# Kernel optimization log

Measured on AMD Instinct MI355X. Metric: run time of the kernel, lower is better.

Reference implementation:

```python
import jax, jax.numpy as jnp
import numpy as np
import math

EPS = 1e-8
DIM, HEADS, K = 256, 8, 16
HD = DIM // HEADS
B, N, PDIM = 4, 4096, 3


def _layernorm(x, w, b, eps=1e-5):
    m = jnp.mean(x, axis=-1, keepdims=True)
    v = jnp.mean((x - m) ** 2, axis=-1, keepdims=True)
    return (x - m) * jax.lax.rsqrt(v + eps) * w + b


def setup_inputs() -> dict:
    key = jax.random.key(0)
    ks = jax.random.split(key, 16)
    s = 0.02
    d = {
        'x': jax.random.normal(ks[0], (B, N, DIM), jnp.float32),
        'positions': jax.random.uniform(ks[1], (B, N, PDIM), jnp.float32) * 0.5,  # inside unit ball
        'c': jnp.ones((1,), jnp.float32),
        'time_emb': jax.random.normal(ks[2], (B, DIM), jnp.float32),
        'Wq': jax.random.normal(ks[3], (DIM, DIM), jnp.float32) * s,
        'bq': jnp.zeros((DIM,), jnp.float32),
        'Wk': jax.random.normal(ks[4], (DIM, DIM), jnp.float32) * s,
        'bk': jnp.zeros((DIM,), jnp.float32),
        'Wv': jax.random.normal(ks[5], (DIM, DIM), jnp.float32) * s,
        'bv': jnp.zeros((DIM,), jnp.float32),
        'Wo': jax.random.normal(ks[6], (DIM, DIM), jnp.float32) * s,
        'bo': jnp.zeros((DIM,), jnp.float32),
        'W1': jax.random.normal(ks[7], (DIM, 4 * DIM), jnp.float32) * s,
        'b1': jnp.zeros((4 * DIM,), jnp.float32),
        'W2': jax.random.normal(ks[8], (4 * DIM, DIM), jnp.float32) * s,
        'b2': jnp.zeros((DIM,), jnp.float32),
        'ln1_w': jnp.ones((DIM,), jnp.float32),
        'ln1_b': jnp.zeros((DIM,), jnp.float32),
        'ln2_w': jnp.ones((DIM,), jnp.float32),
        'ln2_b': jnp.zeros((DIM,), jnp.float32),
        'log_tau': jnp.zeros((), jnp.float32),
    }
    return d


def _poincare_dist_matrix(pos, c):
    # pos: [B,N,P], c: scalar > 0. Returns [B,N,N] with d[b,i,j] = dist(pos[b,j], pos[b,i])
    sq = jnp.sum(pos ** 2, axis=-1)                      # [B,N]
    diff2 = (sq[:, :, None] + sq[:, None, :]
             - 2.0 * jnp.einsum('bip,bjp->bij', pos, pos))
    diff2 = jnp.maximum(diff2, 0.0)
    num = 2.0 * c * diff2
    den = (1.0 - c * sq[:, :, None]) * (1.0 - c * sq[:, None, :])
    arg = jnp.maximum(1.0 + num / (den + EPS), 1.0)
    return jnp.arccosh(arg) / jnp.sqrt(c)


def reference(x, positions, c, time_emb, Wq, bq, Wk, bk, Wv, bv, Wo, bo,
              W1, b1, W2, b2, ln1_w, ln1_b, ln2_w, ln2_b, log_tau):
    c_s = jnp.squeeze(c)
    x_res = x
    h = _layernorm(x, ln1_w, ln1_b) + time_emb[:, None, :]

    q = (h @ Wq + bq).reshape(B, N, HEADS, HD).transpose(0, 2, 1, 3)  # [B,H,N,hd]
    k = (h @ Wk + bk).reshape(B, N, HEADS, HD).transpose(0, 2, 1, 3)
    v = (h @ Wv + bv).reshape(B, N, HEADS, HD).transpose(0, 2, 1, 3)

    # pairwise hyperbolic distances + kNN (no_grad in original)
    dist = jax.lax.stop_gradient(_poincare_dist_matrix(positions, c_s))  # [B,N,N]
    neg_vals, idx = jax.lax.top_k(-dist, K)          # smallest-K distances
    attn_dists = -neg_vals                            # [B,N,K]

    # gather neighbor keys/values: out[b,h,n,j,d] = k[b,h,idx[b,n,j],d]
    idx_flat = idx.reshape(B, 1, N * K, 1)            # broadcast over heads, hd
    k_g = jnp.take_along_axis(k, idx_flat, axis=2).reshape(B, HEADS, N, K, HD)
    v_g = jnp.take_along_axis(v, idx_flat, axis=2).reshape(B, HEADS, N, K, HD)

    feat = jnp.einsum('bhnd,bhnkd->bhnk', q, k_g) / math.sqrt(HD)
    tau = jnp.exp(log_tau) + EPS
    scores = feat - attn_dists[:, None, :, :] / tau
    probs = jax.nn.softmax(scores, axis=-1)
    attn = jnp.einsum('bhnk,bhnkd->bhnd', probs, v_g)
    attn = attn.transpose(0, 2, 1, 3).reshape(B, N, DIM)

    x2 = x_res + attn @ Wo + bo
    ff = jax.nn.gelu(_layernorm(x2, ln2_w, ln2_b) @ W1 + b1, approximate=False) @ W2 + b2
    return x2 + ff
```

## Files before the change

### kernel.cpp

```cpp
#include <hip/hip_runtime.h>
#include <math.h>

namespace {

constexpr int kBatch = 4;
constexpr int kN = 4096;
constexpr int kDim = 256;
constexpr int kHeads = 8;
constexpr int kK = 16;
constexpr float kEps = 1e-8f;

using u16 = unsigned short;
typedef __attribute__((ext_vector_type(8))) short short8;
typedef __attribute__((ext_vector_type(8))) u16 u16x8;
typedef __attribute__((ext_vector_type(4))) float f32x4;

__device__ __forceinline__ float b2f(u16 u) {
  union { unsigned int i; float f; } x; x.i = ((unsigned int)u) << 16; return x.f;
}
__device__ __forceinline__ u16 f2b(float f) {
  union { float f; unsigned int i; } x; x.f = f;
  unsigned int r = x.i + 0x7fffu + ((x.i >> 16) & 1u);
  return (u16)(r >> 16);
}
__device__ __forceinline__ float gelu_exact(float x) {
  return 0.5f * x * (1.0f + erff(x * 0.70710678118654752f));
}
__device__ __forceinline__ void load_lds16(const u16* g, u16* l) {
  __builtin_amdgcn_global_load_lds(
      (const __attribute__((address_space(1))) unsigned int*)g,
      (__attribute__((address_space(3))) unsigned int*)l, 16, 0, 0);
}

template<bool ADD_TEMB>
__global__ __launch_bounds__(256) void ln_kernel(
    const float* __restrict__ x, const float* __restrict__ w,
    const float* __restrict__ bb, const float* __restrict__ temb,
    u16* __restrict__ out) {
  int gt = blockIdx.x * 256 + threadIdx.x;
  int row = gt >> 6;
  int lane = threadIdx.x & 63;
  const float4* xr = (const float4*)(x + (size_t)row * kDim);
  float4 v = xr[lane];
  float s = v.x + v.y + v.z + v.w;
  #pragma unroll
  for (int off = 32; off; off >>= 1) s += __shfl_xor(s, off);
  float mean = s * (1.0f / kDim);
  float dx = v.x - mean, dy = v.y - mean, dz = v.z - mean, dw = v.w - mean;
  float ss = dx * dx + dy * dy + dz * dz + dw * dw;
  #pragma unroll
  for (int off = 32; off; off >>= 1) ss += __shfl_xor(ss, off);
  float rstd = rsqrtf(ss * (1.0f / kDim) + 1e-5f);
  float4 wv = ((const float4*)w)[lane];
  float4 bv = ((const float4*)bb)[lane];
  float ox = dx * rstd * wv.x + bv.x;
  float oy = dy * rstd * wv.y + bv.y;
  float oz = dz * rstd * wv.z + bv.z;
  float ow = dw * rstd * wv.w + bv.w;
  if (ADD_TEMB) {
    int bi = row >> 12;
    float4 t = ((const float4*)(temb + (size_t)bi * kDim))[lane];
    ox += t.x; oy += t.y; oz += t.z; ow += t.w;
  }
  ushort4 ob;
  ob.x = f2b(ox); ob.y = f2b(oy); ob.z = f2b(oz); ob.w = f2b(ow);
  ((ushort4*)(out + (size_t)row * kDim))[lane] = ob;
}

__global__ __launch_bounds__(256) void wconv_all_kernel(
    const float* __restrict__ Wq, const float* __restrict__ Wk,
    const float* __restrict__ Wv, const float* __restrict__ Wo,
    const float* __restrict__ W1, const float* __restrict__ W2,
    u16* __restrict__ Tq, u16* __restrict__ Tk,
    u16* __restrict__ Tv, u16* __restrict__ To,
    u16* __restrict__ T1, u16* __restrict__ T2) {
  int idx = blockIdx.x * 256 + threadIdx.x;
  int seg = idx >> 18;
  int e = idx & 262143;
  if (seg == 0) {
    int which = e >> 16, ee = e & 65535;
    const float* W = which == 0 ? Wq : which == 1 ? Wk : which == 2 ? Wv : Wo;
    u16* T = which == 0 ? Tq : which == 1 ? Tk : which == 2 ? Tv : To;
    int n = ee >> 8, kk = ee & 255;
    T[ee] = f2b(W[kk * 256 + n]);
  } else if (seg == 1) {
    int n = e >> 8, kk = e & 255;
    T1[e] = f2b(W1[kk * 1024 + n]);
  } else {
    int n = e >> 10, kk = e & 1023;
    T2[e] = f2b(W2[kk * 256 + n]);
  }
}

template<int EPI, int BN>
__device__ __forceinline__ void gemm_body(
    const u16* __restrict__ A, const u16* __restrict__ Bt,
    const float* __restrict__ bias, const float* __restrict__ R,
    float* __restrict__ Cf, u16* __restrict__ Cbf,
    int N, int K, int bx, int by) {
  constexpr int NI = BN / 32;
  __shared__ u16 Al[128 * 32];
  __shared__ u16 Bl[BN * 32];
  int tid = threadIdx.x;
  int wv = tid >> 6, ln = tid & 63;
  int wr = wv >> 1, wc = wv & 1;
  int lhi = ln >> 4, llo = ln & 15;
  int bm = bx * 128, bn = by * BN;

  f32x4 zero = {0.f, 0.f, 0.f, 0.f};
  f32x4 acc[4][NI];
  #pragma unroll
  for (int mi = 0; mi < 4; ++mi)
    #pragma unroll
    for (int ni = 0; ni < NI; ++ni) acc[mi][ni] = zero;

  for (int k0 = 0; k0 < K; k0 += 32) {
    if (k0) __syncthreads();
    #pragma unroll
    for (int i = 0; i < 2; ++i) {
      int f = i * 256 + tid;
      int r = f >> 2, kp = f & 3;
      load_lds16(A + (size_t)(bm + r) * K + k0 + kp * 8,
                 &Al[(i * 256 + wv * 64) * 8]);
    }
    #pragma unroll
    for (int i = 0; i < BN / 64; ++i) {
      int f = i * 256 + tid;
      int r = f >> 2, kp = f & 3;
      load_lds16(Bt + (size_t)(bn + r) * K + k0 + kp * 8,
                 &Bl[(i * 256 + wv * 64) * 8]);
    }
    __syncthreads();
    short8 af[4], bf[NI];
    #pragma unroll
    for (int mi = 0; mi < 4; ++mi)
      af[mi] = *(const short8*)&Al[(wr * 64 + mi * 16 + llo) * 32 + lhi * 8];
    #pragma unroll
    for (int ni = 0; ni < NI; ++ni)
      bf[ni] = *(const short8*)&Bl[(wc * (BN / 2) + ni * 16 + llo) * 32 + lhi * 8];
    #pragma unroll
    for (int mi = 0; mi < 4; ++mi)
      #pragma unroll
      for (int ni = 0; ni < NI; ++ni)
        acc[mi][ni] = __builtin_amdgcn_mfma_f32_16x16x32_bf16(
            af[mi], bf[ni], acc[mi][ni], 0, 0, 0);
  }

  #pragma unroll
  for (int mi = 0; mi < 4; ++mi) {
    #pragma unroll
    for (int r = 0; r < 4; ++r) {
      int row = bm + wr * 64 + mi * 16 + lhi * 4 + r;
      #pragma unroll
      for (int ni = 0; ni < NI; ++ni) {
        int col = bn + wc * (BN / 2) + ni * 16 + llo;
        float val = acc[mi][ni][r] + bias[col];
        if (EPI == 1) {
          val += R[(size_t)row * N + col];
          Cf[(size_t)row * N + col] = val;
        } else {
          if (EPI == 2) val = gelu_exact(val);
          Cbf[(size_t)row * N + col] = f2b(val);
        }
      }
    }
  }
}

template<int EPI, int BN>
__global__ __launch_bounds__(256) void gemm_kernel(
    const u16* __restrict__ A, const u16* __restrict__ Bt,
    const float* __restrict__ bias, const float* __restrict__ R,
    float* __restrict__ Cf, u16* __restrict__ Cbf, int N, int K) {
  gemm_body<EPI, BN>(A, Bt, bias, R, Cf, Cbf, N, K, blockIdx.x, blockIdx.y);
}

__global__ __launch_bounds__(256) void qkv_kernel(
    const u16* __restrict__ A,
    const u16* __restrict__ Bq, const u16* __restrict__ Bk, const u16* __restrict__ Bv,
    const float* __restrict__ bq, const float* __restrict__ bk, const float* __restrict__ bv,
    u16* __restrict__ q, u16* __restrict__ k, u16* __restrict__ v) {
  int sel = blockIdx.y >> 1;
  const u16* Bt = sel == 0 ? Bq : sel == 1 ? Bk : Bv;
  const float* bias = sel == 0 ? bq : sel == 1 ? bk : bv;
  u16* C = sel == 0 ? q : sel == 1 ? k : v;
  gemm_body<0, 128>(A, Bt, bias, nullptr, nullptr, C, 256, 256,
                    blockIdx.x, blockIdx.y & 1);
}

__global__ __launch_bounds__(1024, 4) void topk_kernel(
    const float* __restrict__ pos, const float* __restrict__ cptr,
    int* __restrict__ idx_out, float* __restrict__ dist_out) {
  __shared__ float4 ps[kN];
  int tid = threadIdx.x;
  int wave = tid >> 6, ln = tid & 63;
  int row = blockIdx.x * 16 + wave;
  int b = row >> 12;
  float c = cptr[0];
  const float4* pbv = (const float4*)(pos + (size_t)b * kN * 3);
  {
    int q = tid;
    float4 f0 = pbv[q * 3 + 0], f1 = pbv[q * 3 + 1], f2 = pbv[q * 3 + 2];
    float xs[4] = {f0.x, f0.w, f1.z, f2.y};
    float ys[4] = {f0.y, f1.x, f1.w, f2.z};
    float zs[4] = {f0.z, f1.y, f2.x, f2.w};
    #pragma unroll
    for (int e = 0; e < 4; ++e)
      ps[q * 4 + e] = make_float4(xs[e], ys[e], zs[e],
          c * (xs[e] * xs[e] + ys[e] * ys[e] + zs[e] * zs[e]));
  }
  __syncthreads();

  int i = row & (kN - 1);
  float4 pi = ps[i];
  float wi = pi.w, oi = 1.0f - wi;
  float sx = 2.0f * c * pi.x, sy = 2.0f * c * pi.y, sz = 2.0f * c * pi.z;

  auto pkey = [&](int j) -> unsigned {
    float4 pj = ps[j];
    float tt = wi + pj.w;
    tt = fmaf(-sx, pj.x, tt);
    tt = fmaf(-sy, pj.y, tt);
    tt = fmaf(-sz, pj.z, tt);
    float num = 2.0f * fmaxf(tt, 0.0f);
    float den = fmaf(-oi, pj.w, oi) + kEps;
    float r = num * __builtin_amdgcn_rcpf(den);
    union { float f; unsigned u; } cv; cv.f = r;
    return (cv.u & 0xFFFFF000u) | (unsigned)j;
  };

  unsigned lpk = pkey(ln);
  #pragma unroll
  for (int kk = 2; kk <= 64; kk <<= 1) {
    #pragma unroll
    for (int jj = kk >> 1; jj >= 1; jj >>= 1) {
      unsigned ov = (unsigned)__shfl_xor((int)lpk, jj);
      bool keepMin = (((ln & kk) == 0) == ((ln & jj) == 0));
      bool less = ov < lpk;
      if (keepMin ? less : !less) lpk = ov;
    }
  }
  unsigned T = (unsigned)__builtin_amdgcn_readlane((int)lpk, 15);

  for (int t = 1; t < 64; ++t) {
    unsigned cpk = pkey(ln + t * 64);
    unsigned long long m = __ballot(cpk < T);
    if (m) {
      do {
        int src = __ffsll(m) - 1;
        m &= m - 1;
        unsigned npk = (unsigned)__builtin_amdgcn_readlane((int)cpk, src);
        unsigned pv = (unsigned)__builtin_amdgcn_update_dpp(
            0, (int)lpk, 0x111 , 0xF, 0xF, false);
        bool gt = lpk > npk;
        bool take = gt && ((ln == 0) || (pv <= npk));
        lpk = take ? npk : (gt ? pv : lpk);
      } while (m);
      T = (unsigned)__builtin_amdgcn_readlane((int)lpk, 15);
    }
  }

  if (ln < kK) {
    int j = (int)(lpk & 0xFFFu);
    float4 pj = ps[j];
    float tt = wi + pj.w;
    tt = fmaf(-sx, pj.x, tt);
    tt = fmaf(-sy, pj.y, tt);
    tt = fmaf(-sz, pj.z, tt);
    float num = 2.0f * fmaxf(tt, 0.0f);
    float den = fmaf(-oi, pj.w, oi) + kEps;
    float arg = fmaxf(1.0f + num / den, 1.0f);
    float rs = 1.0f / sqrtf(c);
    idx_out[(size_t)row * kK + ln] = j;
    dist_out[(size_t)row * kK + ln] = acoshf(arg) * rs;
  }
}

__global__ __launch_bounds__(256) void attn_kernel(
    const u16* __restrict__ q, const u16* __restrict__ k,
    const u16* __restrict__ v, const int* __restrict__ nidx,
    const float* __restrict__ ndist, const float* __restrict__ log_tau,
    u16* __restrict__ out) {
  int t = blockIdx.x * 256 + threadIdx.x;
  int h = t & (kHeads - 1);
  int row = t >> 3;
  int b = row >> 12;
  float rtau = 1.0f / (expf(log_tau[0]) + kEps);
  const u16x8* qr = (const u16x8*)(q + (size_t)row * kDim + h * 32);
  float qf[32];
  #pragma unroll
  for (int cch = 0; cch < 4; ++cch) {
    u16x8 u = qr[cch];
    #pragma unroll
    for (int e = 0; e < 8; ++e) qf[cch * 8 + e] = b2f(u[e]);
  }

  int njs[kK];
  float sc[kK];
  const int* ir = nidx + (size_t)row * kK;
  const float* dr = ndist + (size_t)row * kK;
  float smax = -1e30f;
  #pragma unroll
  for (int j = 0; j < kK; ++j) {
    int nj = ir[j];
    njs[j] = nj;
    const u16x8* kr = (const u16x8*)(k + ((size_t)b * kN + nj) * kDim + h * 32);
    float dot = 0.0f;
    #pragma unroll
    for (int cch = 0; cch < 4; ++cch) {
      u16x8 u = kr[cch];
      #pragma unroll
      for (int e = 0; e < 8; ++e) dot = fmaf(qf[cch * 8 + e], b2f(u[e]), dot);
    }
    float s = dot * 0.17677669529663687f - dr[j] * rtau;
    sc[j] = s;
    smax = fmaxf(smax, s);
  }
  float sum = 0.0f;
  #pragma unroll
  for (int j = 0; j < kK; ++j) { sc[j] = expf(sc[j] - smax); sum += sc[j]; }
  float rsum = 1.0f / sum;
  float o[32];
  #pragma unroll
  for (int d = 0; d < 32; ++d) o[d] = 0.0f;
  #pragma unroll
  for (int j = 0; j < kK; ++j) {
    float p = sc[j] * rsum;
    const u16x8* vr = (const u16x8*)(v + ((size_t)b * kN + njs[j]) * kDim + h * 32);
    #pragma unroll
    for (int cch = 0; cch < 4; ++cch) {
      u16x8 u = vr[cch];
      #pragma unroll
      for (int e = 0; e < 8; ++e) o[cch * 8 + e] = fmaf(p, b2f(u[e]), o[cch * 8 + e]);
    }
  }
  u16x8* orow = (u16x8*)(out + (size_t)row * kDim + h * 32);
  #pragma unroll
  for (int cch = 0; cch < 4; ++cch) {
    u16x8 po;
    #pragma unroll
    for (int e = 0; e < 8; ++e) po[e] = f2b(o[cch * 8 + e]);
    orow[cch] = po;
  }
}

}

extern "C" void kernel_launch(void* const* d_in, const int* in_sizes, int n_in,
                              void* d_out, int out_size, void* d_ws, size_t ws_size,
                              hipStream_t stream) {
  const float* x    = (const float*)d_in[0];
  const float* pos  = (const float*)d_in[1];
  const float* c    = (const float*)d_in[2];
  const float* temb = (const float*)d_in[3];
  const float* Wq   = (const float*)d_in[4];
  const float* bq   = (const float*)d_in[5];
  const float* Wk   = (const float*)d_in[6];
  const float* bk   = (const float*)d_in[7];
  const float* Wv   = (const float*)d_in[8];
  const float* bv   = (const float*)d_in[9];
  const float* Wo   = (const float*)d_in[10];
  const float* bo   = (const float*)d_in[11];
  const float* W1   = (const float*)d_in[12];
  const float* b1   = (const float*)d_in[13];
  const float* W2   = (const float*)d_in[14];
  const float* b2   = (const float*)d_in[15];
  const float* ln1w = (const float*)d_in[16];
  const float* ln1b = (const float*)d_in[17];
  const float* ln2w = (const float*)d_in[18];
  const float* ln2b = (const float*)d_in[19];
  const float* ltau = (const float*)d_in[20];

  const size_t MB = 1ull << 20;
  char* w = (char*)d_ws;
  u16*   h_bf  = (u16*)(w + 0 * MB);
  u16*   qb    = (u16*)(w + 8 * MB);
  u16*   kb    = (u16*)(w + 16 * MB);
  u16*   vb    = (u16*)(w + 24 * MB);
  u16*   attnb = (u16*)(w + 32 * MB);
  float* x2    = (float*)(w + 40 * MB);
  u16*   g_bf  = (u16*)(w + 56 * MB);
  u16*   wq_t  = (u16*)(w + 88 * MB);
  u16*   wk_t  = wq_t + 65536;
  u16*   wv_t  = wq_t + 2 * 65536;
  u16*   wo_t  = wq_t + 3 * 65536;
  u16*   w1_t  = (u16*)(w + 89 * MB);
  u16*   w2_t  = (u16*)(w + 89 * MB + 512 * 1024);
  int*   kidx  = (int*)(w + 90 * MB);
  float* kdst  = (float*)(w + 91 * MB);
  u16*   tln   = h_bf;

  hipLaunchKernelGGL(wconv_all_kernel, dim3(3072), dim3(256), 0, stream,
                     Wq, Wk, Wv, Wo, W1, W2, wq_t, wk_t, wv_t, wo_t, w1_t, w2_t);
  hipLaunchKernelGGL((ln_kernel<true>), dim3(4096), dim3(256), 0, stream,
                     x, ln1w, ln1b, temb, h_bf);
  hipLaunchKernelGGL(topk_kernel, dim3(1024), dim3(1024), 0, stream,
                     pos, c, kidx, kdst);
  hipLaunchKernelGGL(qkv_kernel, dim3(128, 6), dim3(256), 0, stream,
                     h_bf, wq_t, wk_t, wv_t, bq, bk, bv, qb, kb, vb);
  hipLaunchKernelGGL(attn_kernel, dim3(512), dim3(256), 0, stream,
                     qb, kb, vb, kidx, kdst, ltau, attnb);
  hipLaunchKernelGGL((gemm_kernel<1, 64>), dim3(128, 4), dim3(256), 0, stream,
                     attnb, wo_t, bo, x, x2, (u16*)nullptr, 256, 256);
  hipLaunchKernelGGL((ln_kernel<false>), dim3(4096), dim3(256), 0, stream,
                     x2, ln2w, ln2b, nullptr, tln);
  hipLaunchKernelGGL((gemm_kernel<2, 128>), dim3(128, 8), dim3(256), 0, stream,
                     tln, w1_t, b1, nullptr, (float*)nullptr, g_bf, 1024, 256);
  hipLaunchKernelGGL((gemm_kernel<1, 64>), dim3(128, 4), dim3(256), 0, stream,
                     g_bf, w2_t, b2, x2, (float*)d_out, (u16*)nullptr, 256, 1024);
}
```

Before: 190.0 us.

## Filter topk candidates with a division-free threshold test and batch ballots

The kNN scan now compares num against a slightly inflated threshold times den, so it skips the reciprocal for candidates that are rejected. It also processes four candidate chunks per iteration to expose more ILP. The exact packed key is computed only for accepted candidates. Separately, the weight conversion now uses a tiled shared-memory transpose for coalesced access, and the position staging is simplified to scalar strided loads.

```diff
diff --git a/kernel.cpp b/kernel.cpp
--- a/kernel.cpp
+++ b/kernel.cpp
@@ -30,6 +30,11 @@
   __builtin_amdgcn_global_load_lds(
       (const __attribute__((address_space(1))) unsigned int*)g,
       (__attribute__((address_space(3))) unsigned int*)l, 16, 0, 0);
+}
+__device__ __forceinline__ float readlane_f(float v, int l) {
+  union { float f; int i; } x; x.f = v;
+  x.i = __builtin_amdgcn_readlane(x.i, l);
+  return x.f;
 }
 
 template<bool ADD_TEMB>
@@ -67,28 +72,38 @@
   ((ushort4*)(out + (size_t)row * kDim))[lane] = ob;
 }
 
-__global__ __launch_bounds__(256) void wconv_all_kernel(
+__global__ __launch_bounds__(256) void wtrans_kernel(
     const float* __restrict__ Wq, const float* __restrict__ Wk,
     const float* __restrict__ Wv, const float* __restrict__ Wo,
     const float* __restrict__ W1, const float* __restrict__ W2,
     u16* __restrict__ Tq, u16* __restrict__ Tk,
     u16* __restrict__ Tv, u16* __restrict__ To,
     u16* __restrict__ T1, u16* __restrict__ T2) {
-  int idx = blockIdx.x * 256 + threadIdx.x;
-  int seg = idx >> 18;
-  int e = idx & 262143;
+  __shared__ float t[32][33];
+  int bx = blockIdx.x;
+  int seg = bx >> 8, e = bx & 255;
+  const float* W; u16* T; int Kin, Nin, kt, nt;
   if (seg == 0) {
-    int which = e >> 16, ee = e & 65535;
-    const float* W = which == 0 ? Wq : which == 1 ? Wk : which == 2 ? Wv : Wo;
-    u16* T = which == 0 ? Tq : which == 1 ? Tk : which == 2 ? Tv : To;
-    int n = ee >> 8, kk = ee & 255;
-    T[ee] = f2b(W[kk * 256 + n]);
+    int which = e >> 6, tl = e & 63;
+    W = which == 0 ? Wq : which == 1 ? Wk : which == 2 ? Wv : Wo;
+    T = which == 0 ? Tq : which == 1 ? Tk : which == 2 ? Tv : To;
+    Kin = 256; Nin = 256; kt = tl >> 3; nt = tl & 7;
   } else if (seg == 1) {
-    int n = e >> 8, kk = e & 255;
-    T1[e] = f2b(W1[kk * 1024 + n]);
+    W = W1; T = T1; Kin = 256; Nin = 1024; kt = e >> 5; nt = e & 31;
   } else {
-    int n = e >> 10, kk = e & 1023;
-    T2[e] = f2b(W2[kk * 256 + n]);
+    W = W2; T = T2; Kin = 1024; Nin = 256; kt = e >> 3; nt = e & 7;
+  }
+  int tx = threadIdx.x & 31, ty = threadIdx.x >> 5;
+  #pragma unroll
+  for (int rr = 0; rr < 4; ++rr) {
+    int r = rr * 8 + ty;
+    t[r][tx] = W[(size_t)(kt * 32 + r) * Nin + nt * 32 + tx];
+  }
+  __syncthreads();
+  #pragma unroll
+  for (int rr = 0; rr < 4; ++rr) {
+    int r = rr * 8 + ty;
+    T[(size_t)(nt * 32 + r) * Kin + kt * 32 + tx] = f2b(t[tx][r]);
   }
 }
 
@@ -197,17 +212,10 @@
   int row = blockIdx.x * 16 + wave;
   int b = row >> 12;
   float c = cptr[0];
-  const float4* pbv = (const float4*)(pos + (size_t)b * kN * 3);
-  {
-    int q = tid;
-    float4 f0 = pbv[q * 3 + 0], f1 = pbv[q * 3 + 1], f2 = pbv[q * 3 + 2];
-    float xs[4] = {f0.x, f0.w, f1.z, f2.y};
-    float ys[4] = {f0.y, f1.x, f1.w, f2.z};
-    float zs[4] = {f0.z, f1.y, f2.x, f2.w};
-    #pragma unroll
-    for (int e = 0; e < 4; ++e)
-      ps[q * 4 + e] = make_float4(xs[e], ys[e], zs[e],
-          c * (xs[e] * xs[e] + ys[e] * ys[e] + zs[e] * zs[e]));
+  const float* pb = pos + (size_t)b * kN * 3;
+  for (int j = tid; j < kN; j += 1024) {
+    float x = pb[j * 3 + 0], y = pb[j * 3 + 1], z = pb[j * 3 + 2];
+    ps[j] = make_float4(x, y, z, c * (x * x + y * y + z * z));
   }
   __syncthreads();
 
@@ -216,20 +224,24 @@
   float wi = pi.w, oi = 1.0f - wi;
   float sx = 2.0f * c * pi.x, sy = 2.0f * c * pi.y, sz = 2.0f * c * pi.z;
 
-  auto pkey = [&](int j) -> unsigned {
+  auto numden = [&](int j, float& num, float& den) {
     float4 pj = ps[j];
     float tt = wi + pj.w;
     tt = fmaf(-sx, pj.x, tt);
     tt = fmaf(-sy, pj.y, tt);
     tt = fmaf(-sz, pj.z, tt);
-    float num = 2.0f * fmaxf(tt, 0.0f);
-    float den = fmaf(-oi, pj.w, oi) + kEps;
+    num = fmaxf(tt, 0.0f);
+    den = fmaf(-oi, pj.w, oi);
+  };
+  auto packkey = [&](float num, float den, int j) -> unsigned {
     float r = num * __builtin_amdgcn_rcpf(den);
     union { float f; unsigned u; } cv; cv.f = r;
     return (cv.u & 0xFFFFF000u) | (unsigned)j;
   };
 
-  unsigned lpk = pkey(ln);
+  float n0, d0;
+  numden(ln, n0, d0);
+  unsigned lpk = packkey(n0, d0, ln);
   #pragma unroll
   for (int kk = 2; kk <= 64; kk <<= 1) {
     #pragma unroll
@@ -241,22 +253,57 @@
     }
   }
   unsigned T = (unsigned)__builtin_amdgcn_readlane((int)lpk, 15);
-
-  for (int t = 1; t < 64; ++t) {
-    unsigned cpk = pkey(ln + t * 64);
-    unsigned long long m = __ballot(cpk < T);
-    if (m) {
-      do {
-        int src = __ffsll(m) - 1;
-        m &= m - 1;
-        unsigned npk = (unsigned)__builtin_amdgcn_readlane((int)cpk, src);
-        unsigned pv = (unsigned)__builtin_amdgcn_update_dpp(
-            0, (int)lpk, 0x111 , 0xF, 0xF, false);
-        bool gt = lpk > npk;
-        bool take = gt && ((ln == 0) || (pv <= npk));
-        lpk = take ? npk : (gt ? pv : lpk);
-      } while (m);
+  float Tf;
+  {
+    union { unsigned u; float f; } tv; tv.u = T & 0xFFFFF000u;
+    Tf = fmaf(tv.f, 0.001f, tv.f);
+  }
+
+  auto insertAll = [&](unsigned long long m, float num, float den, int base) {
+    while (m) {
+      int src = __ffsll(m) - 1;
+      m &= m - 1;
+      float ns = readlane_f(num, src);
+      float ds = readlane_f(den, src);
+      unsigned npk = packkey(ns, ds, base + src);
+      unsigned pv = (unsigned)__builtin_amdgcn_update_dpp(
+          0, (int)lpk, 0x111 , 0xF, 0xF, false);
+      bool gt = lpk > npk;
+      bool take = gt && ((ln == 0) || (pv <= npk));
+      lpk = take ? npk : (gt ? pv : lpk);
+    }
+  };
+
+  int t = 1;
+  for (; t + 3 < 64; t += 4) {
+    float a0, b0, a1, b1, a2, b2, a3, b3;
+    numden(ln + (t + 0) * 64, a0, b0);
+    numden(ln + (t + 1) * 64, a1, b1);
+    numden(ln + (t + 2) * 64, a2, b2);
+    numden(ln + (t + 3) * 64, a3, b3);
+    unsigned long long m0 = __ballot(a0 < Tf * b0);
+    unsigned long long m1 = __ballot(a1 < Tf * b1);
+    unsigned long long m2 = __ballot(a2 < Tf * b2);
+    unsigned long long m3 = __ballot(a3 < Tf * b3);
+    if (m0 | m1 | m2 | m3) {
+      insertAll(m0, a0, b0, (t + 0) * 64);
+      insertAll(m1, a1, b1, (t + 1) * 64);
+      insertAll(m2, a2, b2, (t + 2) * 64);
+      insertAll(m3, a3, b3, (t + 3) * 64);
       T = (unsigned)__builtin_amdgcn_readlane((int)lpk, 15);
+      union { unsigned u; float f; } tv; tv.u = T & 0xFFFFF000u;
+      Tf = fmaf(tv.f, 0.001f, tv.f);
+    }
+  }
+  for (; t < 64; ++t) {
+    float a0, b0;
+    numden(ln + t * 64, a0, b0);
+    unsigned long long m0 = __ballot(a0 < Tf * b0);
+    if (m0) {
+      insertAll(m0, a0, b0, t * 64);
+      T = (unsigned)__builtin_amdgcn_readlane((int)lpk, 15);
+      union { unsigned u; float f; } tv; tv.u = T & 0xFFFFF000u;
+      Tf = fmaf(tv.f, 0.001f, tv.f);
     }
   }
 
@@ -390,7 +437,7 @@
   float* kdst  = (float*)(w + 91 * MB);
   u16*   tln   = h_bf;
 
-  hipLaunchKernelGGL(wconv_all_kernel, dim3(3072), dim3(256), 0, stream,
+  hipLaunchKernelGGL(wtrans_kernel, dim3(768), dim3(256), 0, stream,
                      Wq, Wk, Wv, Wo, W1, W2, wq_t, wk_t, wv_t, wo_t, w1_t, w2_t);
   hipLaunchKernelGGL((ln_kernel<true>), dim3(4096), dim3(256), 0, stream,
                      x, ln1w, ln1b, temb, h_bf);
```

Result: slower. 202.8 us (+6.7%).
